# Kernel tuning notes

Hardware: AMD Instinct MI355X
Metric: run time of the kernel (lower is better)

## Reference

```python
import jax, jax.numpy as jnp
import numpy as np

N_NODES = 50000
N_EDGES = 800000
EMB = 200
HID = 128
OUT = 32
VOCABS = [64, 16, 8]


def setup_inputs() -> dict:
    key = jax.random.key(0)
    ks = jax.random.split(key, 20)
    x = jax.random.randint(ks[0], (N_NODES, 3), 0, 8)
    edge_index = jax.random.randint(ks[1], (2, N_EDGES), 0, N_NODES)
    emb0 = jax.random.normal(ks[2], (VOCABS[0], EMB), jnp.float32) * 0.02
    emb1 = jax.random.normal(ks[3], (VOCABS[1], EMB), jnp.float32) * 0.02
    emb2 = jax.random.normal(ks[4], (VOCABS[2], EMB), jnp.float32) * 0.02
    d_in = 3 * EMB  # concat aggregation -> 600
    def lin(k, fi, fo):
        s = 1.0 / np.sqrt(fi)
        return jax.random.uniform(k, (fi, fo), jnp.float32, -s, s)
    w_rel0, w_root0 = lin(ks[5], d_in, HID), lin(ks[6], d_in, HID)
    b0 = jnp.zeros((HID,), jnp.float32)
    w_rel1, w_root1 = lin(ks[7], HID, HID), lin(ks[8], HID, HID)
    b1 = jnp.zeros((HID,), jnp.float32)
    w_rel2, w_root2 = lin(ks[9], HID, HID), lin(ks[10], HID, HID)
    b2 = jnp.zeros((HID,), jnp.float32)
    w_out = lin(ks[11], HID, OUT)
    b_out = jnp.zeros((OUT,), jnp.float32)
    return {"x": x, "edge_index": edge_index,
            "emb0": emb0, "emb1": emb1, "emb2": emb2,
            "w_rel0": w_rel0, "w_root0": w_root0, "b0": b0,
            "w_rel1": w_rel1, "w_root1": w_root1, "b1": b1,
            "w_rel2": w_rel2, "w_root2": w_root2, "b2": b2,
            "w_out": w_out, "b_out": b_out}


def _graph_conv(X, src, tgt, w_rel, w_root, b):
    # PyG GraphConv(aggr='mean'): out_i = W_rel @ mean_{j->i} x_j + b + W_root @ x_i
    msg = X[src]                                               # [E, d]
    ssum = jax.ops.segment_sum(msg, tgt, num_segments=N_NODES)  # [N, d]
    cnt = jax.ops.segment_sum(jnp.ones((src.shape[0], 1), X.dtype), tgt,
                              num_segments=N_NODES)             # [N, 1]
    agg = ssum / jnp.maximum(cnt, 1.0)
    return agg @ w_rel + b + X @ w_root


def reference(x, edge_index, emb0, emb1, emb2,
              w_rel0, w_root0, b0, w_rel1, w_root1, b1,
              w_rel2, w_root2, b2, w_out, b_out):
    # FeatureEmbedding: per-feature embedding lookup, concat along feature dim
    X = jnp.concatenate([emb0[x[:, 0]], emb1[x[:, 1]], emb2[x[:, 2]]], axis=-1)  # [N, 600]
    src, tgt = edge_index[0], edge_index[1]  # messages flow src -> tgt
    X = jax.nn.elu(_graph_conv(X, src, tgt, w_rel0, w_root0, b0))
    X = jax.nn.elu(_graph_conv(X, src, tgt, w_rel1, w_root1, b1))
    X = jax.nn.elu(_graph_conv(X, src, tgt, w_rel2, w_root2, b2))
    return X @ w_out + b_out  # [N, 32] logits
```

## Files before the change

kernel.cpp:

```cpp
#include <hip/hip_runtime.h>
#include <hip/hip_bf16.h>
#include <math.h>


#define N_NODES 50000
#define N_EDGES 800000
#define SCAN_NBLK ((N_NODES + 255) / 256)

__device__ __forceinline__ float eluf(float v) {
    return v > 0.0f ? v : expm1f(v);
}
__device__ __forceinline__ float b2f(unsigned short u) {
    union { unsigned int i; float f; } v; v.i = ((unsigned int)u) << 16; return v.f;
}
__device__ __forceinline__ unsigned short f2b(float f) {
    union { float f; unsigned int i; } v; v.f = f;
    return (unsigned short)((v.i + 0x7FFFu + ((v.i >> 16) & 1u)) >> 16);
}

__global__ __launch_bounds__(256) void count_combo_kernel(
        const int* __restrict__ tgt, const int* __restrict__ x,
        int* __restrict__ cnt, int* __restrict__ combo, int E) {
    int i = blockIdx.x * 256 + threadIdx.x;
    if (i < E) atomicAdd(&cnt[tgt[i]], 1);
    if (i < N_NODES)
        combo[i] = x[i * 3] * 64 + x[i * 3 + 1] * 8 + x[i * 3 + 2];
}

__global__ __launch_bounds__(256) void scan_part_kernel(const int* __restrict__ cnt,
        int* __restrict__ part) {
    int i = blockIdx.x * 256 + threadIdx.x;
    int v = (i < N_NODES) ? cnt[i] : 0;
    #pragma unroll
    for (int o = 32; o > 0; o >>= 1) v += __shfl_down(v, o, 64);
    __shared__ int ws[4];
    if ((threadIdx.x & 63) == 0) ws[threadIdx.x >> 6] = v;
    __syncthreads();
    if (threadIdx.x == 0) part[blockIdx.x] = ws[0] + ws[1] + ws[2] + ws[3];
}

__global__ __launch_bounds__(256) void scan_top_kernel(int* __restrict__ part) {
    __shared__ int tmp[256];
    int t = threadIdx.x;
    int v = (t < SCAN_NBLK) ? part[t] : 0;
    tmp[t] = v;
    __syncthreads();
    for (int o = 1; o < 256; o <<= 1) {
        int u = (t >= o) ? tmp[t - o] : 0;
        __syncthreads();
        tmp[t] += u;
        __syncthreads();
    }
    if (t < SCAN_NBLK) part[t] = tmp[t] - v;
}

__global__ __launch_bounds__(256) void scan_final_kernel(const int* __restrict__ cnt,
        const int* __restrict__ part, int* __restrict__ offsets, int* __restrict__ pos) {
    __shared__ int tmp[256];
    int i = blockIdx.x * 256 + threadIdx.x;
    int t = threadIdx.x;
    int v = (i < N_NODES) ? cnt[i] : 0;
    tmp[t] = v;
    __syncthreads();
    for (int o = 1; o < 256; o <<= 1) {
        int u = (t >= o) ? tmp[t - o] : 0;
        __syncthreads();
        tmp[t] += u;
        __syncthreads();
    }
    int excl = tmp[t] - v + part[blockIdx.x];
    if (i < N_NODES) { offsets[i] = excl; pos[i] = excl; }
    if (i == 0) offsets[N_NODES] = N_EDGES;
}

__global__ __launch_bounds__(256) void fill_kernel(const int* __restrict__ src,
        const int* __restrict__ tgt, const int* __restrict__ combo,
        int* __restrict__ pos, int* __restrict__ oc) {
    int e = blockIdx.x * 256 + threadIdx.x;
    if (e < N_EDGES) {
        int s = src[e];
        int slot = atomicAdd(&pos[tgt[e]], 1);
        oc[slot] = s | (combo[s] << 16);
    }
}

__global__ __launch_bounds__(256) void ptab_kernel(const float* __restrict__ e0,
        const float* __restrict__ e1, const float* __restrict__ e2,
        const float* __restrict__ wrel, const float* __restrict__ wroot,
        float* __restrict__ P) {
    const int b = blockIdx.x;
    const int t = b >> 3, v = b & 7;
    const float* emb = (t == 0) ? e0 : (t == 1 ? e1 : e2);
    const float* erow = &emb[v * 200];
    const int c = threadIdx.x;
    const float* W = (c < 128) ? wrel : wroot;
    const float* Wp = &W[(size_t)(t * 200) * 128 + (c & 127)];
    __shared__ float es[200];
    for (int k = threadIdx.x; k < 200; k += 256) es[k] = erow[k];
    __syncthreads();
    float a0 = 0.f, a1 = 0.f;
    #pragma unroll 8
    for (int k = 0; k < 200; k += 2) {
        a0 = fmaf(es[k],     Wp[(size_t)k * 128],       a0);
        a1 = fmaf(es[k + 1], Wp[(size_t)(k + 1) * 128], a1);
    }
    P[(size_t)b * 256 + c] = a0 + a1;
}

__global__ __launch_bounds__(256) void ytab_kernel(const float* __restrict__ P,
        unsigned short* __restrict__ Ycb) {
    const int q = blockIdx.x;
    const int c = threadIdx.x;
    const float p0 = P[(size_t)(q >> 6) * 256 + c];
    const float p1 = P[(size_t)(8 + ((q >> 3) & 7)) * 256 + c];
    const float p2 = P[(size_t)(16 + (q & 7)) * 256 + c];
    Ycb[(size_t)q * 256 + c] = f2b(p0 + p1 + p2);
}

__global__ __launch_bounds__(256) void aggregate0_kernel(
        const unsigned short* __restrict__ Ycb, const int* __restrict__ oc,
        const int* __restrict__ combo, const int* __restrict__ offsets,
        const float* __restrict__ b, float* __restrict__ Xn) {
    int idx = blockIdx.x * 256 + threadIdx.x;
    int node = idx >> 5;
    int c = (idx & 31) * 4;
    if (node >= N_NODES) return;
    const int beg = offsets[node], end = offsets[node + 1];
    float ax = 0.f, ay = 0.f, az = 0.f, aw = 0.f;
    float gx = 0.f, gy = 0.f, gz = 0.f, gw = 0.f;
    int j = beg;
    for (; j + 3 < end; j += 4) {
        int q0 = oc[j] >> 16, q1 = oc[j + 1] >> 16;
        int q2 = oc[j + 2] >> 16, q3 = oc[j + 3] >> 16;
        ushort4 u0 = *(const ushort4*)&Ycb[(size_t)q0 * 256 + c];
        ushort4 u1 = *(const ushort4*)&Ycb[(size_t)q1 * 256 + c];
        ushort4 u2 = *(const ushort4*)&Ycb[(size_t)q2 * 256 + c];
        ushort4 u3 = *(const ushort4*)&Ycb[(size_t)q3 * 256 + c];
        ax += b2f(u0.x) + b2f(u1.x); ay += b2f(u0.y) + b2f(u1.y);
        az += b2f(u0.z) + b2f(u1.z); aw += b2f(u0.w) + b2f(u1.w);
        gx += b2f(u2.x) + b2f(u3.x); gy += b2f(u2.y) + b2f(u3.y);
        gz += b2f(u2.z) + b2f(u3.z); gw += b2f(u2.w) + b2f(u3.w);
    }
    for (; j < end; ++j) {
        int q0 = oc[j] >> 16;
        ushort4 u0 = *(const ushort4*)&Ycb[(size_t)q0 * 256 + c];
        ax += b2f(u0.x); ay += b2f(u0.y); az += b2f(u0.z); aw += b2f(u0.w);
    }
    float sx = ax + gx, sy = ay + gy, sz = az + gz, sw = aw + gw;
    const float inv = 1.0f / fmaxf((float)(end - beg), 1.0f);
    ushort4 ur = *(const ushort4*)&Ycb[(size_t)combo[node] * 256 + 128 + c];
    float4 bb = *(const float4*)&b[c];
    float4 o;
    o.x = eluf(fmaf(sx, inv, bb.x) + b2f(ur.x));
    o.y = eluf(fmaf(sy, inv, bb.y) + b2f(ur.y));
    o.z = eluf(fmaf(sz, inv, bb.z) + b2f(ur.z));
    o.w = eluf(fmaf(sw, inv, bb.w) + b2f(ur.w));
    *(float4*)&Xn[(size_t)node * 128 + c] = o;
}

__global__ __launch_bounds__(256) void aggregate_kernel(
        const unsigned short* __restrict__ Ybrel, const float* __restrict__ Yroot,
        const int* __restrict__ oc, const int* __restrict__ offsets,
        const float* __restrict__ b, float* __restrict__ Xn) {
    int idx = blockIdx.x * 256 + threadIdx.x;
    int node = idx >> 5;
    int c = (idx & 31) * 4;
    if (node >= N_NODES) return;
    const int beg = offsets[node], end = offsets[node + 1];
    float ax = 0.f, ay = 0.f, az = 0.f, aw = 0.f;
    float gx = 0.f, gy = 0.f, gz = 0.f, gw = 0.f;
    int j = beg;
    for (; j + 3 < end; j += 4) {
        int s0 = oc[j] & 0xFFFF, s1 = oc[j + 1] & 0xFFFF;
        int s2 = oc[j + 2] & 0xFFFF, s3 = oc[j + 3] & 0xFFFF;
        ushort4 u0 = *(const ushort4*)&Ybrel[(size_t)s0 * 128 + c];
        ushort4 u1 = *(const ushort4*)&Ybrel[(size_t)s1 * 128 + c];
        ushort4 u2 = *(const ushort4*)&Ybrel[(size_t)s2 * 128 + c];
        ushort4 u3 = *(const ushort4*)&Ybrel[(size_t)s3 * 128 + c];
        ax += b2f(u0.x) + b2f(u1.x); ay += b2f(u0.y) + b2f(u1.y);
        az += b2f(u0.z) + b2f(u1.z); aw += b2f(u0.w) + b2f(u1.w);
        gx += b2f(u2.x) + b2f(u3.x); gy += b2f(u2.y) + b2f(u3.y);
        gz += b2f(u2.z) + b2f(u3.z); gw += b2f(u2.w) + b2f(u3.w);
    }
    for (; j < end; ++j) {
        int s0 = oc[j] & 0xFFFF;
        ushort4 u0 = *(const ushort4*)&Ybrel[(size_t)s0 * 128 + c];
        ax += b2f(u0.x); ay += b2f(u0.y); az += b2f(u0.z); aw += b2f(u0.w);
    }
    float sx = ax + gx, sy = ay + gy, sz = az + gz, sw = aw + gw;
    const float inv = 1.0f / fmaxf((float)(end - beg), 1.0f);
    float4 yr = *(const float4*)&Yroot[(size_t)node * 128 + c];
    float4 bb = *(const float4*)&b[c];
    float4 o;
    o.x = eluf(fmaf(sx, inv, bb.x) + yr.x);
    o.y = eluf(fmaf(sy, inv, bb.y) + yr.y);
    o.z = eluf(fmaf(sz, inv, bb.z) + yr.z);
    o.w = eluf(fmaf(sw, inv, bb.w) + yr.w);
    *(float4*)&Xn[(size_t)node * 128 + c] = o;
}

__global__ __launch_bounds__(256) void conv_kernel(const float* __restrict__ Yf,
        unsigned short* __restrict__ Yb) {
    int i = blockIdx.x * 256 + threadIdx.x;
    if (i >= N_NODES * 16) return;
    float4 a = ((const float4*)Yf)[(size_t)i * 2];
    float4 b = ((const float4*)Yf)[(size_t)i * 2 + 1];
    uint4 w;
    w.x = (unsigned int)f2b(a.x) | ((unsigned int)f2b(a.y) << 16);
    w.y = (unsigned int)f2b(a.z) | ((unsigned int)f2b(a.w) << 16);
    w.z = (unsigned int)f2b(b.x) | ((unsigned int)f2b(b.y) << 16);
    w.w = (unsigned int)f2b(b.z) | ((unsigned int)f2b(b.w) << 16);
    ((uint4*)Yb)[i] = w;
}

template<int K>
__global__ __launch_bounds__(256, 4) void gemm_rr(
        const float* __restrict__ A,
        const float* __restrict__ Brel, const float* __restrict__ Broot,
        float* __restrict__ Yrel, float* __restrict__ Yroot, int M) {
    __shared__ float As[8][132];
    __shared__ float Bs[8][132];
    const float* __restrict__ B = (blockIdx.y == 0) ? Brel : Broot;
    float* __restrict__ Yp = (blockIdx.y == 0) ? Yrel : Yroot;
    const int m0 = blockIdx.x * 128;
    const int tid = threadIdx.x;
    const int am = tid & 127, ak = (tid >> 7) * 4;
    const int bc = (tid & 31) * 4, bk = tid >> 5;
    const int tr = (tid >> 4) * 8, tc = (tid & 15) * 8;
    const int arow = min(m0 + am, M - 1);
    float acc[8][8] = {};

    float4 av = *(const float4*)&A[(size_t)arow * K + ak];
    float4 bv = *(const float4*)&B[(size_t)bk * 128 + bc];

    for (int kt = 0; kt < K; kt += 8) {
        __syncthreads();
        As[ak + 0][am] = av.x;
        As[ak + 1][am] = av.y;
        As[ak + 2][am] = av.z;
        As[ak + 3][am] = av.w;
        *(float4*)&Bs[bk][bc] = bv;
        __syncthreads();
        if (kt + 8 < K) {
            av = *(const float4*)&A[(size_t)arow * K + kt + 8 + ak];
            bv = *(const float4*)&B[(size_t)(kt + 8 + bk) * 128 + bc];
        }
        #pragma unroll
        for (int kk = 0; kk < 8; ++kk) {
            float a[8], b[8];
            *(float4*)&a[0] = *(const float4*)&As[kk][tr];
            *(float4*)&a[4] = *(const float4*)&As[kk][tr + 4];
            *(float4*)&b[0] = *(const float4*)&Bs[kk][tc];
            *(float4*)&b[4] = *(const float4*)&Bs[kk][tc + 4];
            #pragma unroll
            for (int i = 0; i < 8; ++i)
                #pragma unroll
                for (int j = 0; j < 8; ++j)
                    acc[i][j] = fmaf(a[i], b[j], acc[i][j]);
        }
    }
    #pragma unroll
    for (int i = 0; i < 8; ++i) {
        int row = m0 + tr + i;
        if (row < M) {
            *(float4*)&Yp[(size_t)row * 128 + tc] =
                make_float4(acc[i][0], acc[i][1], acc[i][2], acc[i][3]);
            *(float4*)&Yp[(size_t)row * 128 + tc + 4] =
                make_float4(acc[i][4], acc[i][5], acc[i][6], acc[i][7]);
        }
    }
}

__global__ __launch_bounds__(256) void out_kernel(const float* __restrict__ X,
        const float* __restrict__ W, const float* __restrict__ bo,
        float* __restrict__ out, int M) {
    __shared__ float Ws[128 * 32];
    const int tid = threadIdx.x;
    #pragma unroll
    for (int o = tid * 4; o < 4096; o += 1024)
        *(float4*)&Ws[o] = *(const float4*)&W[o];
    __syncthreads();
    const int row = blockIdx.x * 32 + (tid >> 3);
    const int col = (tid & 7) * 4;
    if (row >= M) return;
    float a0 = 0.f, a1 = 0.f, a2 = 0.f, a3 = 0.f;
    for (int k4 = 0; k4 < 32; ++k4) {
        float4 xv = *(const float4*)&X[(size_t)row * 128 + k4 * 4];
        float xa[4] = {xv.x, xv.y, xv.z, xv.w};
        #pragma unroll
        for (int j = 0; j < 4; ++j) {
            float4 wv = *(const float4*)&Ws[(k4 * 4 + j) * 32 + col];
            a0 = fmaf(xa[j], wv.x, a0);
            a1 = fmaf(xa[j], wv.y, a1);
            a2 = fmaf(xa[j], wv.z, a2);
            a3 = fmaf(xa[j], wv.w, a3);
        }
    }
    float4 bb = *(const float4*)&bo[col];
    *(float4*)&out[(size_t)row * 32 + col] =
        make_float4(a0 + bb.x, a1 + bb.y, a2 + bb.z, a3 + bb.w);
}

extern "C" void kernel_launch(void* const* d_in, const int* in_sizes, int n_in,
                              void* d_out, int out_size, void* d_ws, size_t ws_size,
                              hipStream_t stream) {
    const int* x        = (const int*)d_in[0];
    const int* ei       = (const int*)d_in[1];
    const float* e0     = (const float*)d_in[2];
    const float* e1     = (const float*)d_in[3];
    const float* e2     = (const float*)d_in[4];
    const float* w_rel0 = (const float*)d_in[5];
    const float* w_root0= (const float*)d_in[6];
    const float* b0     = (const float*)d_in[7];
    const float* w_rel1 = (const float*)d_in[8];
    const float* w_root1= (const float*)d_in[9];
    const float* b1     = (const float*)d_in[10];
    const float* w_rel2 = (const float*)d_in[11];
    const float* w_root2= (const float*)d_in[12];
    const float* b2     = (const float*)d_in[13];
    const float* w_out  = (const float*)d_in[14];
    const float* b_out  = (const float*)d_in[15];
    float* out = (float*)d_out;

    const int N = N_NODES, E = N_EDGES;
    char* base = (char*)d_ws;
    float*          F0  = (float*)base;
    float*          F1  = (float*)(base + 25600000);
    float*          F2  = (float*)(base + 51200000);
    unsigned short* H   = (unsigned short*)(base + 76800000);
    int*            oc  = (int*)(base + 89600000);
    float*          P   = (float*)(base + 92800000);
    unsigned short* Ycb = (unsigned short*)(base + 92824576);
    int*            cnt     = (int*)(base + 93086720);
    int*            offsets = cnt + N;
    int*            pos     = offsets + N + 1;
    int*            combo   = pos + N;
    int*            part    = combo + N;

    const int* src = ei;
    const int* tgt = ei + E;

    hipMemsetAsync(cnt, 0, N * sizeof(int), stream);
    count_combo_kernel<<<(E + 255) / 256, 256, 0, stream>>>(tgt, x, cnt, combo, E);
    scan_part_kernel<<<SCAN_NBLK, 256, 0, stream>>>(cnt, part);
    scan_top_kernel<<<1, 256, 0, stream>>>(part);
    scan_final_kernel<<<SCAN_NBLK, 256, 0, stream>>>(cnt, part, offsets, pos);
    fill_kernel<<<(E + 255) / 256, 256, 0, stream>>>(src, tgt, combo, pos, oc);

    ptab_kernel<<<24, 256, 0, stream>>>(e0, e1, e2, w_rel0, w_root0, P);
    ytab_kernel<<<512, 256, 0, stream>>>(P, Ycb);

    const int agg_grid = (N * 32 + 255) / 256;
    const int conv_grid = (N * 16 + 255) / 256;
    dim3 ggrid((N + 127) / 128, 2);

    aggregate0_kernel<<<agg_grid, 256, 0, stream>>>(Ycb, oc, combo, offsets, b0, F0);

    gemm_rr<128><<<ggrid, 256, 0, stream>>>(F0, w_rel1, w_root1, F2, F1, N);
    conv_kernel<<<conv_grid, 256, 0, stream>>>(F2, H);
    aggregate_kernel<<<agg_grid, 256, 0, stream>>>(H, F1, oc, offsets, b1, F2);

    gemm_rr<128><<<ggrid, 256, 0, stream>>>(F2, w_rel2, w_root2, F0, F1, N);
    conv_kernel<<<conv_grid, 256, 0, stream>>>(F0, H);
    aggregate_kernel<<<agg_grid, 256, 0, stream>>>(H, F1, oc, offsets, b2, F0);

    out_kernel<<<(N + 31) / 32, 256, 0, stream>>>(F0, w_out, b_out, out, N);
}
```

Baseline: 420.9 us.

## Replace FP32 SIMT GEMM with bf16 MFMA GEMM and store activations as bf16

Replaces the shared-memory FP32 FMA GEMM for layers 1 and 2 with a matrix-core kernel using 16x16x32 bf16 MFMA. Weights are pre-packed into the MFMA operand layout by a new pack kernel. The aggregate kernels now write bf16 node features, which halves activation traffic into the GEMM and the output layer. This lowers precision of intermediate activations, and the GEMM output stores are scalar and strided rather than vectorised.

```diff
diff --git a/kernel.cpp b/kernel.cpp
--- a/kernel.cpp
+++ b/kernel.cpp
@@ -6,6 +6,9 @@
 #define N_NODES 50000
 #define N_EDGES 800000
 #define SCAN_NBLK ((N_NODES + 255) / 256)
+
+typedef __attribute__((ext_vector_type(8))) short bf16x8;
+typedef __attribute__((ext_vector_type(4))) float f32x4;
 
 __device__ __forceinline__ float eluf(float v) {
     return v > 0.0f ? v : expm1f(v);
@@ -117,10 +120,69 @@
     Ycb[(size_t)q * 256 + c] = f2b(p0 + p1 + p2);
 }
 
+__global__ __launch_bounds__(64) void pack_kernel(const float* __restrict__ w1r,
+        const float* __restrict__ w1t, const float* __restrict__ w2r,
+        const float* __restrict__ w2t, unsigned short* __restrict__ Bp) {
+    const int b = blockIdx.x, l = threadIdx.x;
+    const int mat = b >> 5, ks = (b >> 3) & 3, ct = b & 7;
+    const float* W = (mat == 0) ? w1r : (mat == 1) ? w1t : (mat == 2) ? w2r : w2t;
+    const int col = ct * 16 + (l & 15);
+    const int krow = ks * 32 + 8 * (l >> 4);
+    unsigned short v[8];
+    #pragma unroll
+    for (int i = 0; i < 8; ++i)
+        v[i] = f2b(W[(size_t)(krow + i) * 128 + col]);
+    unsigned short* dst = &Bp[(size_t)((((mat * 4 + ks) * 8 + ct) * 64 + l) * 8)];
+    #pragma unroll
+    for (int i = 0; i < 8; ++i) dst[i] = v[i];
+}
+
+__global__ __launch_bounds__(256) void gemm_mfma(
+        const unsigned short* __restrict__ Xb, const unsigned short* __restrict__ Bp,
+        int matbase, float* __restrict__ Yrel, float* __restrict__ Yroot, int M) {
+    const int plane = blockIdx.y;
+    const unsigned short* Bpm = Bp + (size_t)(matbase + plane) * 4 * 8 * 64 * 8;
+    float* __restrict__ Yp = plane ? Yroot : Yrel;
+    const int w = threadIdx.x >> 6;
+    const int l = threadIdx.x & 63;
+    const int rbase = blockIdx.x * 128 + w * 32;
+    const int arow0 = min(rbase + (l & 15), M - 1);
+    const int arow1 = min(rbase + 16 + (l & 15), M - 1);
+    const int kl = 8 * (l >> 4);
+    f32x4 acc[2][8] = {};
+    #pragma unroll
+    for (int ks = 0; ks < 4; ++ks) {
+        const int k0 = ks * 32 + kl;
+        bf16x8 a0 = *(const bf16x8*)&Xb[(size_t)arow0 * 128 + k0];
+        bf16x8 a1 = *(const bf16x8*)&Xb[(size_t)arow1 * 128 + k0];
+        const unsigned short* bbase = Bpm + (size_t)ks * 8 * 64 * 8 + (size_t)l * 8;
+        #pragma unroll
+        for (int ct = 0; ct < 8; ++ct) {
+            bf16x8 bf = *(const bf16x8*)&bbase[(size_t)ct * 64 * 8];
+            acc[0][ct] = __builtin_amdgcn_mfma_f32_16x16x32_bf16(a0, bf, acc[0][ct], 0, 0, 0);
+            acc[1][ct] = __builtin_amdgcn_mfma_f32_16x16x32_bf16(a1, bf, acc[1][ct], 0, 0, 0);
+        }
+    }
+    const int colb = l & 15;
+    const int rowoff = (l >> 4) * 4;
+    #pragma unroll
+    for (int rt = 0; rt < 2; ++rt) {
+        #pragma unroll
+        for (int j = 0; j < 4; ++j) {
+            const int row = rbase + rt * 16 + rowoff + j;
+            if (row < M) {
+                #pragma unroll
+                for (int ct = 0; ct < 8; ++ct)
+                    Yp[(size_t)row * 128 + ct * 16 + colb] = acc[rt][ct][j];
+            }
+        }
+    }
+}
+
 __global__ __launch_bounds__(256) void aggregate0_kernel(
         const unsigned short* __restrict__ Ycb, const int* __restrict__ oc,
         const int* __restrict__ combo, const int* __restrict__ offsets,
-        const float* __restrict__ b, float* __restrict__ Xn) {
+        const float* __restrict__ b, unsigned short* __restrict__ Xn) {
     int idx = blockIdx.x * 256 + threadIdx.x;
     int node = idx >> 5;
     int c = (idx & 31) * 4;
@@ -150,18 +212,18 @@
     const float inv = 1.0f / fmaxf((float)(end - beg), 1.0f);
     ushort4 ur = *(const ushort4*)&Ycb[(size_t)combo[node] * 256 + 128 + c];
     float4 bb = *(const float4*)&b[c];
-    float4 o;
-    o.x = eluf(fmaf(sx, inv, bb.x) + b2f(ur.x));
-    o.y = eluf(fmaf(sy, inv, bb.y) + b2f(ur.y));
-    o.z = eluf(fmaf(sz, inv, bb.z) + b2f(ur.z));
-    o.w = eluf(fmaf(sw, inv, bb.w) + b2f(ur.w));
-    *(float4*)&Xn[(size_t)node * 128 + c] = o;
+    ushort4 o;
+    o.x = f2b(eluf(fmaf(sx, inv, bb.x) + b2f(ur.x)));
+    o.y = f2b(eluf(fmaf(sy, inv, bb.y) + b2f(ur.y)));
+    o.z = f2b(eluf(fmaf(sz, inv, bb.z) + b2f(ur.z)));
+    o.w = f2b(eluf(fmaf(sw, inv, bb.w) + b2f(ur.w)));
+    *(ushort4*)&Xn[(size_t)node * 128 + c] = o;
 }
 
 __global__ __launch_bounds__(256) void aggregate_kernel(
         const unsigned short* __restrict__ Ybrel, const float* __restrict__ Yroot,
         const int* __restrict__ oc, const int* __restrict__ offsets,
-        const float* __restrict__ b, float* __restrict__ Xn) {
+        const float* __restrict__ b, unsigned short* __restrict__ Xn) {
     int idx = blockIdx.x * 256 + threadIdx.x;
     int node = idx >> 5;
     int c = (idx & 31) * 4;
@@ -191,12 +253,12 @@
     const float inv = 1.0f / fmaxf((float)(end - beg), 1.0f);
     float4 yr = *(const float4*)&Yroot[(size_t)node * 128 + c];
     float4 bb = *(const float4*)&b[c];
-    float4 o;
-    o.x = eluf(fmaf(sx, inv, bb.x) + yr.x);
-    o.y = eluf(fmaf(sy, inv, bb.y) + yr.y);
-    o.z = eluf(fmaf(sz, inv, bb.z) + yr.z);
-    o.w = eluf(fmaf(sw, inv, bb.w) + yr.w);
-    *(float4*)&Xn[(size_t)node * 128 + c] = o;
+    ushort4 o;
+    o.x = f2b(eluf(fmaf(sx, inv, bb.x) + yr.x));
+    o.y = f2b(eluf(fmaf(sy, inv, bb.y) + yr.y));
+    o.z = f2b(eluf(fmaf(sz, inv, bb.z) + yr.z));
+    o.w = f2b(eluf(fmaf(sw, inv, bb.w) + yr.w));
+    *(ushort4*)&Xn[(size_t)node * 128 + c] = o;
 }
 
 __global__ __launch_bounds__(256) void conv_kernel(const float* __restrict__ Yf,
@@ -213,65 +275,7 @@
     ((uint4*)Yb)[i] = w;
 }
 
-template<int K>
-__global__ __launch_bounds__(256, 4) void gemm_rr(
-        const float* __restrict__ A,
-        const float* __restrict__ Brel, const float* __restrict__ Broot,
-        float* __restrict__ Yrel, float* __restrict__ Yroot, int M) {
-    __shared__ float As[8][132];
-    __shared__ float Bs[8][132];
-    const float* __restrict__ B = (blockIdx.y == 0) ? Brel : Broot;
-    float* __restrict__ Yp = (blockIdx.y == 0) ? Yrel : Yroot;
-    const int m0 = blockIdx.x * 128;
-    const int tid = threadIdx.x;
-    const int am = tid & 127, ak = (tid >> 7) * 4;
-    const int bc = (tid & 31) * 4, bk = tid >> 5;
-    const int tr = (tid >> 4) * 8, tc = (tid & 15) * 8;
-    const int arow = min(m0 + am, M - 1);
-    float acc[8][8] = {};
-
-    float4 av = *(const float4*)&A[(size_t)arow * K + ak];
-    float4 bv = *(const float4*)&B[(size_t)bk * 128 + bc];
-
-    for (int kt = 0; kt < K; kt += 8) {
-        __syncthreads();
-        As[ak + 0][am] = av.x;
-        As[ak + 1][am] = av.y;
-        As[ak + 2][am] = av.z;
-        As[ak + 3][am] = av.w;
-        *(float4*)&Bs[bk][bc] = bv;
-        __syncthreads();
-        if (kt + 8 < K) {
-            av = *(const float4*)&A[(size_t)arow * K + kt + 8 + ak];
-            bv = *(const float4*)&B[(size_t)(kt + 8 + bk) * 128 + bc];
-        }
-        #pragma unroll
-        for (int kk = 0; kk < 8; ++kk) {
-            float a[8], b[8];
-            *(float4*)&a[0] = *(const float4*)&As[kk][tr];
-            *(float4*)&a[4] = *(const float4*)&As[kk][tr + 4];
-            *(float4*)&b[0] = *(const float4*)&Bs[kk][tc];
-            *(float4*)&b[4] = *(const float4*)&Bs[kk][tc + 4];
-            #pragma unroll
-            for (int i = 0; i < 8; ++i)
-                #pragma unroll
-                for (int j = 0; j < 8; ++j)
-                    acc[i][j] = fmaf(a[i], b[j], acc[i][j]);
-        }
-    }
-    #pragma unroll
-    for (int i = 0; i < 8; ++i) {
-        int row = m0 + tr + i;
-        if (row < M) {
-            *(float4*)&Yp[(size_t)row * 128 + tc] =
-                make_float4(acc[i][0], acc[i][1], acc[i][2], acc[i][3]);
-            *(float4*)&Yp[(size_t)row * 128 + tc + 4] =
-                make_float4(acc[i][4], acc[i][5], acc[i][6], acc[i][7]);
-        }
-    }
-}
-
-__global__ __launch_bounds__(256) void out_kernel(const float* __restrict__ X,
+__global__ __launch_bounds__(256) void out_kernel(const unsigned short* __restrict__ X,
         const float* __restrict__ W, const float* __restrict__ bo,
         float* __restrict__ out, int M) {
     __shared__ float Ws[128 * 32];
@@ -284,12 +288,14 @@
     const int col = (tid & 7) * 4;
     if (row >= M) return;
     float a0 = 0.f, a1 = 0.f, a2 = 0.f, a3 = 0.f;
-    for (int k4 = 0; k4 < 32; ++k4) {
-        float4 xv = *(const float4*)&X[(size_t)row * 128 + k4 * 4];
-        float xa[4] = {xv.x, xv.y, xv.z, xv.w};
+    for (int k8 = 0; k8 < 16; ++k8) {
+        ushort4 xl = *(const ushort4*)&X[(size_t)row * 128 + k8 * 8];
+        ushort4 xh = *(const ushort4*)&X[(size_t)row * 128 + k8 * 8 + 4];
+        float xa[8] = {b2f(xl.x), b2f(xl.y), b2f(xl.z), b2f(xl.w),
+                       b2f(xh.x), b2f(xh.y), b2f(xh.z), b2f(xh.w)};
         #pragma unroll
-        for (int j = 0; j < 4; ++j) {
-            float4 wv = *(const float4*)&Ws[(k4 * 4 + j) * 32 + col];
+        for (int j = 0; j < 8; ++j) {
+            float4 wv = *(const float4*)&Ws[(k8 * 8 + j) * 32 + col];
             a0 = fmaf(xa[j], wv.x, a0);
             a1 = fmaf(xa[j], wv.y, a1);
             a2 = fmaf(xa[j], wv.z, a2);
@@ -324,14 +330,15 @@
 
     const int N = N_NODES, E = N_EDGES;
     char* base = (char*)d_ws;
-    float*          F0  = (float*)base;
-    float*          F1  = (float*)(base + 25600000);
-    float*          F2  = (float*)(base + 51200000);
-    unsigned short* H   = (unsigned short*)(base + 76800000);
-    int*            oc  = (int*)(base + 89600000);
-    float*          P   = (float*)(base + 92800000);
-    unsigned short* Ycb = (unsigned short*)(base + 92824576);
-    int*            cnt     = (int*)(base + 93086720);
+    float*          Yrel = (float*)base;
+    float*          Yroot= (float*)(base + 25600000);
+    unsigned short* Xb   = (unsigned short*)(base + 51200000);
+    unsigned short* H    = (unsigned short*)(base + 64000000);
+    int*            oc   = (int*)(base + 76800000);
+    unsigned short* Bp   = (unsigned short*)(base + 80000000);
+    float*          P    = (float*)(base + 80131072);
+    unsigned short* Ycb  = (unsigned short*)(base + 80155648);
+    int*            cnt     = (int*)(base + 80417792);
     int*            offsets = cnt + N;
     int*            pos     = offsets + N + 1;
     int*            combo   = pos + N;
@@ -349,20 +356,21 @@
 
     ptab_kernel<<<24, 256, 0, stream>>>(e0, e1, e2, w_rel0, w_root0, P);
     ytab_kernel<<<512, 256, 0, stream>>>(P, Ycb);
+    pack_kernel<<<128, 64, 0, stream>>>(w_rel1, w_root1, w_rel2, w_root2, Bp);
 
     const int agg_grid = (N * 32 + 255) / 256;
     const int conv_grid = (N * 16 + 255) / 256;
     dim3 ggrid((N + 127) / 128, 2);
 
-    aggregate0_kernel<<<agg_grid, 256, 0, stream>>>(Ycb, oc, combo, offsets, b0, F0);
-
-    gemm_rr<128><<<ggrid, 256, 0, stream>>>(F0, w_rel1, w_root1, F2, F1, N);
-    conv_kernel<<<conv_grid, 256, 0, stream>>>(F2, H);
-    aggregate_kernel<<<agg_grid, 256, 0, stream>>>(H, F1, oc, offsets, b1, F2);
-
-    gemm_rr<128><<<ggrid, 256, 0, stream>>>(F2, w_rel2, w_root2, F0, F1, N);
-    conv_kernel<<<conv_grid, 256, 0, stream>>>(F0, H);
-    aggregate_kernel<<<agg_grid, 256, 0, stream>>>(H, F1, oc, offsets, b2, F0);
-
-    out_kernel<<<(N + 31) / 32, 256, 0, stream>>>(F0, w_out, b_out, out, N);
-}
+    aggregate0_kernel<<<agg_grid, 256, 0, stream>>>(Ycb, oc, combo, offsets, b0, Xb);
+
+    gemm_mfma<<<ggrid, 256, 0, stream>>>(Xb, Bp, 0, Yrel, Yroot, N);
+    conv_kernel<<<conv_grid, 256, 0, stream>>>(Yrel, H);
+    aggregate_kernel<<<agg_grid, 256, 0, stream>>>(H, Yroot, oc, offsets, b1, Xb);
+
+    gemm_mfma<<<ggrid, 256, 0, stream>>>(Xb, Bp, 2, Yrel, Yroot, N);
+    conv_kernel<<<conv_grid, 256, 0, stream>>>(Yrel, H);
+    aggregate_kernel<<<agg_grid, 256, 0, stream>>>(H, Yroot, oc, offsets, b2, Xb);
+
+    out_kernel<<<(N + 31) / 32, 256, 0, stream>>>(Xb, w_out, b_out, out, N);
+}
```

Result: faster. 351.6 us (-16.5%).
